# Kernel optimization log

Hardware: AMD Instinct MI355X
Metric: run time of the kernel (lower is better)

The kernel has to match this reference:

```python
import jax, jax.numpy as jnp
import numpy as np

N_NODES = 50000
N_EDGES = 800000
N_HIDDEN = 64
N_LAYER = 3
IN_DIM = 4


def setup_inputs() -> dict:
    key = jax.random.key(0)
    ks = jax.random.split(key, 10)
    x = jax.random.normal(ks[0], (N_NODES, IN_DIM), dtype=jnp.float32)
    edge_index = jax.random.randint(ks[1], (2, N_EDGES), 0, N_NODES, dtype=jnp.int64)
    # Glorot-style params matching pyg GCNConv (lin has no bias; conv adds bias after aggregation)
    def glorot(k, fan_in, fan_out):
        s = jnp.sqrt(6.0 / (fan_in + fan_out))
        return jax.random.uniform(k, (fan_in, fan_out), jnp.float32, -s, s)
    W_in = glorot(ks[2], IN_DIM, N_HIDDEN)
    b_in = jnp.zeros((N_HIDDEN,), jnp.float32)
    W_h = jnp.stack([glorot(jax.random.fold_in(ks[3], i), N_HIDDEN, N_HIDDEN) for i in range(N_LAYER)])
    b_h = jnp.zeros((N_LAYER, N_HIDDEN), jnp.float32)
    W_out = glorot(ks[4], N_HIDDEN, 1)
    b_out = jnp.zeros((1,), jnp.float32)
    return {"x": x, "edge_index": edge_index, "W_in": W_in, "b_in": b_in,
            "W_h": W_h, "b_h": b_h, "W_out": W_out, "b_out": b_out}


def _gcn_norm(edge_index, n_nodes):
    # add self-loops, compute symmetric norm D^{-1/2} (A+I) D^{-1/2}
    loop = jnp.arange(n_nodes, dtype=edge_index.dtype)
    src = jnp.concatenate([edge_index[0], loop])
    dst = jnp.concatenate([edge_index[1], loop])
    deg = jax.ops.segment_sum(jnp.ones_like(dst, dtype=jnp.float32), dst, num_segments=n_nodes)
    dinv = jax.lax.rsqrt(deg)  # deg >= 1 due to self-loops
    norm = dinv[src] * dinv[dst]
    return src, dst, norm


def _gcn_conv(x, W, b, src, dst, norm, n_nodes):
    h = x @ W                                   # [N, out]
    msg = h[src] * norm[:, None]                # gather + scale, [E+N, out]
    out = jax.ops.segment_sum(msg, dst, num_segments=n_nodes)  # scatter-add
    return out + b


def reference(x, edge_index, W_in, b_in, W_h, b_h, W_out, b_out):
    n = x.shape[0]
    src, dst, norm = _gcn_norm(edge_index, n)
    h = jax.nn.relu(_gcn_conv(x, W_in, b_in, src, dst, norm, n))
    for i in range(W_h.shape[0]):
        h = jax.nn.relu(_gcn_conv(h, W_h[i], b_h[i], src, dst, norm, n))
    return _gcn_conv(h, W_out, b_out, src, dst, norm, n)
```

## Files before the change

kernel.cpp:

```cpp
#include <hip/hip_runtime.h>
#include <hip/hip_bf16.h>


#define TPB 256
#define EPT 8
#define CHUNK (TPB * EPT)
typedef __hip_bfloat16 bf16;
#define B2F __bfloat162float

__global__ void k_zero_cnt(int* __restrict__ cnt, int n) {
    int i = blockIdx.x * blockDim.x + threadIdx.x;
    if (i < n) cnt[i] = 0;
}

__global__ void k_hist(const int* __restrict__ dst, int* __restrict__ cnt, int E, int n) {
    int e = blockIdx.x * blockDim.x + threadIdx.x;
    if (e < E) {
        int d = dst[e];
        if ((unsigned)d < (unsigned)n) atomicAdd(&cnt[d], 1);
    }
}

__global__ void k_blocksum(const int* __restrict__ cnt, int* __restrict__ bsum, int n) {
    __shared__ int s[TPB];
    int i = blockIdx.x * TPB + threadIdx.x;
    s[threadIdx.x] = (i < n) ? cnt[i] : 0;
    __syncthreads();
    for (int off = TPB / 2; off > 0; off >>= 1) {
        if (threadIdx.x < off) s[threadIdx.x] += s[threadIdx.x + off];
        __syncthreads();
    }
    if (threadIdx.x == 0) bsum[blockIdx.x] = s[0];
}

__global__ void k_scan_bsum(int* __restrict__ bsum, int nb) {
    __shared__ int s[TPB];
    int t = threadIdx.x;
    int v = (t < nb) ? bsum[t] : 0;
    s[t] = v;
    __syncthreads();
    for (int off = 1; off < TPB; off <<= 1) {
        int u = (t >= off) ? s[t - off] : 0;
        __syncthreads();
        s[t] += u;
        __syncthreads();
    }
    if (t < nb) bsum[t] = s[t] - v;
}

__global__ void k_scan_final(const int* __restrict__ cnt, const int* __restrict__ bsum,
                             int* __restrict__ row_start, int* __restrict__ cursor,
                             float* __restrict__ dinv, int n) {
    __shared__ int s[TPB];
    int t = threadIdx.x;
    int i = blockIdx.x * TPB + t;
    int v = (i < n) ? cnt[i] : 0;
    s[t] = v;
    __syncthreads();
    for (int off = 1; off < TPB; off <<= 1) {
        int u = (t >= off) ? s[t - off] : 0;
        __syncthreads();
        s[t] += u;
        __syncthreads();
    }
    if (i < n) {
        int excl = bsum[blockIdx.x] + s[t] - v;
        row_start[i] = excl;
        cursor[i] = excl;
        dinv[i] = rsqrtf((float)v + 1.0f);
        if (i == n - 1) row_start[n] = excl + v;
    }
}

__global__ void k_init_bcur(const int* __restrict__ row_start, int* __restrict__ bcur,
                            int B, int n) {
    int b = threadIdx.x;
    if (b < B) bcur[b] = row_start[min(b << 8, n)];
}

__global__ __launch_bounds__(TPB) void k_bin(
    const int* __restrict__ src, const int* __restrict__ dst,
    int* __restrict__ bcur, unsigned* __restrict__ staging, int E, int n) {
    __shared__ int hcnt[256];
    __shared__ int hbase[256];
    int tid = threadIdx.x;
    int e0 = blockIdx.x * CHUNK;
    hcnt[tid] = 0;
    __syncthreads();

    int eb[EPT];
    unsigned rec[EPT];
#pragma unroll
    for (int u = 0; u < EPT; ++u) {
        int e = e0 + u * TPB + tid;
        eb[u] = -1;
        if (e < E) {
            int d = dst[e], s = src[e];
            if ((unsigned)d < (unsigned)n && (unsigned)s < (unsigned)n) {
                eb[u] = d >> 8;
                rec[u] = (unsigned)s | ((unsigned)(d & 255) << 16);
                atomicAdd(&hcnt[eb[u]], 1);
            }
        }
    }
    __syncthreads();
    int c = hcnt[tid];
    hbase[tid] = (c > 0) ? atomicAdd(&bcur[tid], c) : 0;
    hcnt[tid] = 0;
    __syncthreads();
#pragma unroll
    for (int u = 0; u < EPT; ++u) {
        if (eb[u] >= 0) {
            int r = atomicAdd(&hcnt[eb[u]], 1);
            int pos = hbase[eb[u]] + r;
            if ((unsigned)pos < (unsigned)E) staging[pos] = rec[u];
        }
    }
}

__global__ __launch_bounds__(TPB) void k_unbin(
    const unsigned* __restrict__ staging, const int* __restrict__ row_start,
    int* __restrict__ cursor, unsigned short* __restrict__ bucket, int E, int n) {
    int b = blockIdx.x;
    int lo = row_start[min(b << 8, n)];
    int hi = row_start[min((b + 1) << 8, n)];
    lo = max(0, min(lo, E)); hi = max(lo, min(hi, E));
    for (int i = lo + threadIdx.x; i < hi; i += TPB) {
        unsigned r = staging[i];
        int d = min((b << 8) + (int)(r >> 16), n - 1);
        int pos = atomicAdd(&cursor[d], 1);
        if ((unsigned)pos < (unsigned)E) bucket[pos] = (unsigned short)(r & 0xffffu);
    }
}

__global__ void k_mm_in(const float* __restrict__ x, const float* __restrict__ W,
                        const float* __restrict__ dinv, bf16* __restrict__ g, int n) {
    int t = blockIdx.x * blockDim.x + threadIdx.x;
    if (t >= n * 64) return;
    int i = t >> 6, j = t & 63;
    float acc = 0.f;
#pragma unroll
    for (int k = 0; k < 4; ++k) acc = fmaf(x[i * 4 + k], W[k * 64 + j], acc);
    g[t] = __float2bfloat16(acc * dinv[i]);
}

__device__ __forceinline__ void acc_quad(float4& a, uint2 w) {
    a.x += __uint_as_float(w.x << 16);
    a.y += __uint_as_float(w.x & 0xffff0000u);
    a.z += __uint_as_float(w.y << 16);
    a.w += __uint_as_float(w.y & 0xffff0000u);
}

__device__ __forceinline__ void agg_row_quad(const bf16* __restrict__ g,
                                             const unsigned short* __restrict__ bucket,
                                             int k0, int k1, int d, float* __restrict__ sVp,
                                             int lane, unsigned nm1, unsigned Em1) {
    int grp = lane >> 4, i = lane & 15;
    float4 a = {0.f, 0.f, 0.f, 0.f};
    if (grp == 0) {
        uint2 w = *(const uint2*)(g + (size_t)d * 64 + 4 * i);
        acc_quad(a, w);
    }
    for (int base = k0; base < k1; base += 64) {
        int cnt = min(64, k1 - base);
        int rec = bucket[min((unsigned)(base + lane), Em1)];
        int k = 0;
        for (; k + 16 <= cnt; k += 16) {
            unsigned s0 = min((unsigned)__shfl(rec, k + 0 + grp), nm1);
            unsigned s1 = min((unsigned)__shfl(rec, k + 4 + grp), nm1);
            unsigned s2 = min((unsigned)__shfl(rec, k + 8 + grp), nm1);
            unsigned s3 = min((unsigned)__shfl(rec, k + 12 + grp), nm1);
            uint2 w0 = *(const uint2*)(g + (size_t)s0 * 64 + 4 * i);
            uint2 w1 = *(const uint2*)(g + (size_t)s1 * 64 + 4 * i);
            uint2 w2 = *(const uint2*)(g + (size_t)s2 * 64 + 4 * i);
            uint2 w3 = *(const uint2*)(g + (size_t)s3 * 64 + 4 * i);
            acc_quad(a, w0); acc_quad(a, w1); acc_quad(a, w2); acc_quad(a, w3);
        }
        for (; k < cnt; k += 4) {
            int e = k + grp;
            unsigned s = min((unsigned)__shfl(rec, min(e, 63)), nm1);
            uint2 w = *(const uint2*)(g + (size_t)s * 64 + 4 * i);
            if (e < cnt) acc_quad(a, w);
        }
    }
    ((float4*)(sVp + grp * 64))[i] = a;
}

__global__ __launch_bounds__(TPB) void k_gconv(
    const bf16* __restrict__ gIn, const float* __restrict__ dinv,
    const int* __restrict__ row_start, const unsigned short* __restrict__ bucket,
    const float* __restrict__ bias, const float* __restrict__ W,
    bf16* __restrict__ gOut, int n, int E) {
    __shared__ float sW[64 * 64];
    __shared__ float sVp[4][4 * 64];
    int tid = threadIdx.x;
    for (int k = tid; k < 1024; k += TPB) ((float4*)sW)[k] = ((const float4*)W)[k];
    __syncthreads();
    int r = tid >> 6, j = tid & 63;
    int d = blockIdx.x * 4 + r;
    if (d >= n) return;
    float dd = dinv[d];
    int k0 = row_start[d], k1 = row_start[d + 1];
    k1 = min(k1, E); k0 = max(min(k0, k1), 0);
    agg_row_quad(gIn, bucket, k0, k1, d, sVp[r], j, (unsigned)(n - 1), (unsigned)(E - 1));
    float v = sVp[r][j] + sVp[r][64 + j] + sVp[r][128 + j] + sVp[r][192 + j];
    float a = fmaxf(fmaf(dd, v, bias[j]), 0.f);
    sVp[r][j] = a;
    const float4* ap = (const float4*)&sVp[r][0];
    float acc = 0.f;
#pragma unroll
    for (int k4 = 0; k4 < 16; ++k4) {
        float4 a4 = ap[k4];
        acc = fmaf(a4.x, sW[(4 * k4 + 0) * 64 + j], acc);
        acc = fmaf(a4.y, sW[(4 * k4 + 1) * 64 + j], acc);
        acc = fmaf(a4.z, sW[(4 * k4 + 2) * 64 + j], acc);
        acc = fmaf(a4.w, sW[(4 * k4 + 3) * 64 + j], acc);
    }
    gOut[(size_t)d * 64 + j] = __float2bfloat16(acc * dd);
}

__global__ __launch_bounds__(TPB) void k_gconv_z(
    const bf16* __restrict__ gIn, const float* __restrict__ dinv,
    const int* __restrict__ row_start, const unsigned short* __restrict__ bucket,
    const float* __restrict__ bias, const float* __restrict__ Wout,
    float* __restrict__ zg, int n, int E) {
    __shared__ float sVp[4][4 * 64];
    int tid = threadIdx.x;
    int r = tid >> 6, j = tid & 63;
    int d = blockIdx.x * 4 + r;
    if (d >= n) return;
    float dd = dinv[d];
    int k0 = row_start[d], k1 = row_start[d + 1];
    k1 = min(k1, E); k0 = max(min(k0, k1), 0);
    agg_row_quad(gIn, bucket, k0, k1, d, sVp[r], j, (unsigned)(n - 1), (unsigned)(E - 1));
    float v = sVp[r][j] + sVp[r][64 + j] + sVp[r][128 + j] + sVp[r][192 + j];
    float a = fmaxf(fmaf(dd, v, bias[j]), 0.f) * Wout[j];
#pragma unroll
    for (int off = 32; off > 0; off >>= 1) a += __shfl_down(a, off);
    if (j == 0) zg[d] = a * dd;
}

__global__ __launch_bounds__(TPB) void k_out(
    const float* __restrict__ zg, const float* __restrict__ dinv,
    const int* __restrict__ row_start, const unsigned short* __restrict__ bucket,
    const float* __restrict__ b_out, float* __restrict__ out, int n, int E) {
    int t = blockIdx.x * blockDim.x + threadIdx.x;
    int d = t >> 6, lane = t & 63;
    if (d >= n) return;
    int k0 = row_start[d], k1 = row_start[d + 1];
    k1 = min(k1, E); k0 = max(min(k0, k1), 0);
    unsigned nm1 = (unsigned)(n - 1);
    float v = 0.f;
    for (int k = k0 + lane; k < k1; k += 64) {
        unsigned s = min((unsigned)bucket[k], nm1);
        v += zg[s];
    }
#pragma unroll
    for (int off = 32; off > 0; off >>= 1) v += __shfl_down(v, off);
    if (lane == 0) out[d] = fmaf(zg[d] + v, dinv[d], b_out[0]);
}

extern "C" void kernel_launch(void* const* d_in, const int* in_sizes, int n_in,
                              void* d_out, int out_size, void* d_ws, size_t ws_size,
                              hipStream_t stream) {
    const float* x     = (const float*)d_in[0];
    const int*   ei    = (const int*)d_in[1];
    const float* W_in  = (const float*)d_in[2];
    const float* b_in  = (const float*)d_in[3];
    const float* W_h   = (const float*)d_in[4];
    const float* b_h   = (const float*)d_in[5];
    const float* W_out = (const float*)d_in[6];
    const float* b_out = (const float*)d_in[7];
    float* out = (float*)d_out;

    int N = in_sizes[0] / 4;
    int E = in_sizes[1] / 2;
    const int* src = ei;
    const int* dst = ei + E;

    char* ws = (char*)d_ws;
    bf16* gA               = (bf16*)ws;           ws += (size_t)N * 64 * 2;
    bf16* gB               = (bf16*)ws;           ws += (size_t)N * 64 * 2;
    unsigned short* bucket = (unsigned short*)ws; ws += (size_t)E * 2;
    unsigned* staging      = (unsigned*)ws;       ws += (size_t)E * 4;
    int*  row_start        = (int*)ws;            ws += (size_t)(N + 1) * 4;
    int*  cursor           = (int*)ws;            ws += (size_t)N * 4;
    int*  cnt              = (int*)ws;            ws += (size_t)N * 4;
    float* dinv            = (float*)ws;          ws += (size_t)N * 4;
    float* zg              = (float*)ws;          ws += (size_t)N * 4;
    int*  bsum             = (int*)ws;            ws += 257 * 4;
    int*  bcur             = (int*)ws;

    int B   = (N + 255) >> 8;
    int gN  = (N + TPB - 1) / TPB;
    int gE  = (E + TPB - 1) / TPB;
    int gNF = (N * 64 + TPB - 1) / TPB;
    int gN4 = (N + 3) / 4;
    int gBin = (E + CHUNK - 1) / CHUNK;

    k_zero_cnt<<<gN, TPB, 0, stream>>>(cnt, N);
    k_hist<<<gE, TPB, 0, stream>>>(dst, cnt, E, N);
    k_blocksum<<<gN, TPB, 0, stream>>>(cnt, bsum, N);
    k_scan_bsum<<<1, TPB, 0, stream>>>(bsum, gN);
    k_scan_final<<<gN, TPB, 0, stream>>>(cnt, bsum, row_start, cursor, dinv, N);
    k_init_bcur<<<1, TPB, 0, stream>>>(row_start, bcur, B, N);
    k_bin<<<gBin, TPB, 0, stream>>>(src, dst, bcur, staging, E, N);
    k_unbin<<<B, TPB, 0, stream>>>(staging, row_start, cursor, bucket, E, N);

    k_mm_in<<<gNF, TPB, 0, stream>>>(x, W_in, dinv, gA, N);
    k_gconv<<<gN4, TPB, 0, stream>>>(gA, dinv, row_start, bucket, b_in, W_h, gB, N, E);
    k_gconv<<<gN4, TPB, 0, stream>>>(gB, dinv, row_start, bucket, b_h, W_h + 4096, gA, N, E);
    k_gconv<<<gN4, TPB, 0, stream>>>(gA, dinv, row_start, bucket, b_h + 64, W_h + 8192, gB, N, E);
    k_gconv_z<<<gN4, TPB, 0, stream>>>(gB, dinv, row_start, bucket, b_h + 128, W_out, zg, N, E);
    k_out<<<gN4, TPB, 0, stream>>>(zg, dinv, row_start, bucket, b_out, out, N, E);
}
```

Before: 321.7 us.

## Gather neighbor rows via global_load_lds DMA into LDS staging buffers

Replaces the register-based neighbor gather (16 lanes × 8-byte loads, four edges per wave step) with direct global-to-LDS loads of 4 bytes per lane, two edges per wave instruction, staged in a per-row LDS buffer. It then waits on vmcnt and accumulates from LDS. The aim is to cut VGPR pressure and issue the loads asynchronously. In exchange, loads become narrower, each 16-edge chunk needs a full wait, and the extra LDS round-trip and smaller per-load width may reduce memory-level parallelism.

```diff
diff --git a/kernel.cpp b/kernel.cpp
--- a/kernel.cpp
+++ b/kernel.cpp
@@ -7,6 +7,9 @@
 #define CHUNK (TPB * EPT)
 typedef __hip_bfloat16 bf16;
 #define B2F __bfloat162float
+
+__device__ __forceinline__ float bflo(unsigned u) { return __uint_as_float(u << 16); }
+__device__ __forceinline__ float bfhi(unsigned u) { return __uint_as_float(u & 0xffff0000u); }
 
 __global__ void k_zero_cnt(int* __restrict__ cnt, int n) {
     int i = blockIdx.x * blockDim.x + threadIdx.x;
@@ -144,46 +147,42 @@
     g[t] = __float2bfloat16(acc * dinv[i]);
 }
 
-__device__ __forceinline__ void acc_quad(float4& a, uint2 w) {
-    a.x += __uint_as_float(w.x << 16);
-    a.y += __uint_as_float(w.x & 0xffff0000u);
-    a.z += __uint_as_float(w.y << 16);
-    a.w += __uint_as_float(w.y & 0xffff0000u);
-}
-
-__device__ __forceinline__ void agg_row_quad(const bf16* __restrict__ g,
-                                             const unsigned short* __restrict__ bucket,
-                                             int k0, int k1, int d, float* __restrict__ sVp,
-                                             int lane, unsigned nm1, unsigned Em1) {
-    int grp = lane >> 4, i = lane & 15;
-    float4 a = {0.f, 0.f, 0.f, 0.f};
-    if (grp == 0) {
-        uint2 w = *(const uint2*)(g + (size_t)d * 64 + 4 * i);
-        acc_quad(a, w);
-    }
+__device__ __forceinline__ void agg_row_dma(const bf16* __restrict__ g,
+                                            const unsigned short* __restrict__ bucket,
+                                            int k0, int k1, int d,
+                                            char* __restrict__ bufw,
+                                            float* __restrict__ sVrow,
+                                            int lane, unsigned nm1, unsigned Em1) {
+    int h = lane >> 5, w = lane & 31;
+    unsigned us = *(const unsigned*)((const char*)g + (size_t)d * 128 + 4 * w);
+    float ax = 0.f, ay = 0.f;
+    if (h == 0) { ax += bflo(us); ay += bfhi(us); }
     for (int base = k0; base < k1; base += 64) {
-        int cnt = min(64, k1 - base);
+        int bcnt = min(64, k1 - base);
         int rec = bucket[min((unsigned)(base + lane), Em1)];
-        int k = 0;
-        for (; k + 16 <= cnt; k += 16) {
-            unsigned s0 = min((unsigned)__shfl(rec, k + 0 + grp), nm1);
-            unsigned s1 = min((unsigned)__shfl(rec, k + 4 + grp), nm1);
-            unsigned s2 = min((unsigned)__shfl(rec, k + 8 + grp), nm1);
-            unsigned s3 = min((unsigned)__shfl(rec, k + 12 + grp), nm1);
-            uint2 w0 = *(const uint2*)(g + (size_t)s0 * 64 + 4 * i);
-            uint2 w1 = *(const uint2*)(g + (size_t)s1 * 64 + 4 * i);
-            uint2 w2 = *(const uint2*)(g + (size_t)s2 * 64 + 4 * i);
-            uint2 w3 = *(const uint2*)(g + (size_t)s3 * 64 + 4 * i);
-            acc_quad(a, w0); acc_quad(a, w1); acc_quad(a, w2); acc_quad(a, w3);
+        for (int c = 0; c < bcnt; c += 16) {
+            int ccnt = min(16, bcnt - c);
+            int tcount = (ccnt + 1) >> 1;
+            for (int t = 0; t < tcount; ++t) {
+                int idx = c + 2 * t + h;
+                unsigned s = min((unsigned)__shfl(rec, min(idx, 63)), nm1);
+                const char* gp = (const char*)g + (size_t)s * 128 + 4 * w;
+                __builtin_amdgcn_global_load_lds(
+                    (const __attribute__((address_space(1))) void*)gp,
+                    (__attribute__((address_space(3))) void*)(bufw + t * 256),
+                    4, 0, 0);
+            }
+            __builtin_amdgcn_s_waitcnt(0x0f70);
+            for (int t = 0; t < tcount; ++t) {
+                unsigned u = *(const unsigned*)(bufw + t * 256 + 4 * lane);
+                int e = base + c + 2 * t + h;
+                if (e < k1) { ax += bflo(u); ay += bfhi(u); }
+            }
         }
-        for (; k < cnt; k += 4) {
-            int e = k + grp;
-            unsigned s = min((unsigned)__shfl(rec, min(e, 63)), nm1);
-            uint2 w = *(const uint2*)(g + (size_t)s * 64 + 4 * i);
-            if (e < cnt) acc_quad(a, w);
-        }
-    }
-    ((float4*)(sVp + grp * 64))[i] = a;
+    }
+    ax += __shfl_xor(ax, 32);
+    ay += __shfl_xor(ay, 32);
+    if (h == 0) ((float2*)sVrow)[w] = make_float2(ax, ay);
 }
 
 __global__ __launch_bounds__(TPB) void k_gconv(
@@ -192,7 +191,8 @@
     const float* __restrict__ bias, const float* __restrict__ W,
     bf16* __restrict__ gOut, int n, int E) {
     __shared__ float sW[64 * 64];
-    __shared__ float sVp[4][4 * 64];
+    __shared__ unsigned sBuf[4][512];
+    __shared__ float sV[4][64];
     int tid = threadIdx.x;
     for (int k = tid; k < 1024; k += TPB) ((float4*)sW)[k] = ((const float4*)W)[k];
     __syncthreads();
@@ -202,11 +202,11 @@
     float dd = dinv[d];
     int k0 = row_start[d], k1 = row_start[d + 1];
     k1 = min(k1, E); k0 = max(min(k0, k1), 0);
-    agg_row_quad(gIn, bucket, k0, k1, d, sVp[r], j, (unsigned)(n - 1), (unsigned)(E - 1));
-    float v = sVp[r][j] + sVp[r][64 + j] + sVp[r][128 + j] + sVp[r][192 + j];
-    float a = fmaxf(fmaf(dd, v, bias[j]), 0.f);
-    sVp[r][j] = a;
-    const float4* ap = (const float4*)&sVp[r][0];
+    agg_row_dma(gIn, bucket, k0, k1, d, (char*)sBuf[r], sV[r], j,
+                (unsigned)(n - 1), (unsigned)(E - 1));
+    float a = fmaxf(fmaf(dd, sV[r][j], bias[j]), 0.f);
+    sV[r][j] = a;
+    const float4* ap = (const float4*)&sV[r][0];
     float acc = 0.f;
 #pragma unroll
     for (int k4 = 0; k4 < 16; ++k4) {
@@ -224,7 +224,8 @@
     const int* __restrict__ row_start, const unsigned short* __restrict__ bucket,
     const float* __restrict__ bias, const float* __restrict__ Wout,
     float* __restrict__ zg, int n, int E) {
-    __shared__ float sVp[4][4 * 64];
+    __shared__ unsigned sBuf[4][512];
+    __shared__ float sV[4][64];
     int tid = threadIdx.x;
     int r = tid >> 6, j = tid & 63;
     int d = blockIdx.x * 4 + r;
@@ -232,9 +233,9 @@
     float dd = dinv[d];
     int k0 = row_start[d], k1 = row_start[d + 1];
     k1 = min(k1, E); k0 = max(min(k0, k1), 0);
-    agg_row_quad(gIn, bucket, k0, k1, d, sVp[r], j, (unsigned)(n - 1), (unsigned)(E - 1));
-    float v = sVp[r][j] + sVp[r][64 + j] + sVp[r][128 + j] + sVp[r][192 + j];
-    float a = fmaxf(fmaf(dd, v, bias[j]), 0.f) * Wout[j];
+    agg_row_dma(gIn, bucket, k0, k1, d, (char*)sBuf[r], sV[r], j,
+                (unsigned)(n - 1), (unsigned)(E - 1));
+    float a = fmaxf(fmaf(dd, sV[r][j], bias[j]), 0.f) * Wout[j];
 #pragma unroll
     for (int off = 32; off > 0; off >>= 1) a += __shfl_down(a, off);
     if (j == 0) zg[d] = a * dd;
```

Result: slower. 359.8 us (+11.8%).
